# Optimization experiments

Measured on AMD Instinct MI355X. Metric: run time of the kernel, lower is better.

The kernel has to match this reference:

```python
import jax, jax.numpy as jnp
import numpy as np

N = 50000          # nodes
E = 1_600_000      # edges (avg degree 32)
F_IN = 256
F_OUT = 256
ALPHA = 0.2        # LeakyReLU negative slope


def setup_inputs() -> dict:
    key = jax.random.key(0)
    ks = jax.random.split(key, 7)
    x = jax.random.normal(ks[0], (N, F_IN), dtype=jnp.float32)
    row = jax.random.randint(ks[1], (E,), 0, N, dtype=jnp.int32)  # dst i
    col = jax.random.randint(ks[2], (E,), 0, N, dtype=jnp.int32)  # src j
    W_w = jax.random.normal(ks[3], (F_IN, F_OUT), dtype=jnp.float32) / np.sqrt(F_IN).astype(np.float32)
    W_b = jax.random.normal(ks[4], (F_OUT,), dtype=jnp.float32) * 0.01
    a_w = jax.random.normal(ks[5], (2 * F_OUT,), dtype=jnp.float32) / np.sqrt(2 * F_OUT).astype(np.float32)
    a_b = jax.random.normal(ks[6], (1,), dtype=jnp.float32) * 0.01
    return {"x": x, "W_w": W_w, "W_b": W_b, "a_w": a_w, "a_b": a_b,
            "row": row, "col": col}


def reference(x, W_w, W_b, a_w, a_b, row, col):
    # Wh = W(x): [N, F_OUT]
    Wh = x @ W_w + W_b
    # e[i,j] = leakyrelu(a1 . Wh[j] + a2 . Wh[i] + b)
    # (repeat puts Wh[j] in the first half of the concat, repeat_interleave Wh[i] in the second)
    f_dst_part = Wh @ a_w[:F_OUT]   # contribution of column node j
    f_row_part = Wh @ a_w[F_OUT:]   # contribution of row node i
    e = f_dst_part[col] + f_row_part[row] + a_b[0]          # [E]
    e = jnp.where(e > 0, e, ALPHA * e)                      # LeakyReLU
    # sparse softmax over dim=1 (segment = row i), adjacency values are 1.0
    m = jax.ops.segment_max(e, row, num_segments=N)         # [N]
    ex = jnp.exp(e - m[row])
    denom = jax.ops.segment_sum(ex, row, num_segments=N)    # [N]
    att = ex / denom[row]                                   # [E]
    # h'[i] = sum_j att[i,j] * Wh[j]  (spmm), empty rows stay zero
    h_prime = jax.ops.segment_sum(att[:, None] * Wh[col], row, num_segments=N)
    return jax.nn.relu(h_prime)
```

## Files before the change

### kernel.cpp

```cpp
#include <hip/hip_runtime.h>
#include <math.h>

#define N_NODES 50000
#define N_EDGES 1600000
#define F 256
#define ALPHA 0.2f
#define NP 50048
#define NB 196
#define CAP 10240
#define EPB 4096
#define NAB ((N_EDGES + EPB - 1) / EPB)
#define UNROLL 16
#define GEMM_BLOCKS 782
#define FVEC_SLOTS 2048

typedef short bf16x8 __attribute__((ext_vector_type(8)));
typedef float f32x4 __attribute__((ext_vector_type(4)));
typedef _Float16 half4 __attribute__((ext_vector_type(4)));

__device__ __forceinline__ unsigned short f2bf(float f) {
  union { float f; unsigned u; } v; v.f = f;
  unsigned u = v.u;
  return (unsigned short)((u + 0x7fffu + ((u >> 16) & 1u)) >> 16);
}

__device__ __forceinline__ unsigned short f2h_bits(float f) {
  union { _Float16 h; unsigned short u; } v;
  v.h = (_Float16)f;
  return v.u;
}

__device__ __forceinline__ float h_bits2f(unsigned short u) {
  union { _Float16 h; unsigned short u; } v;
  v.u = u;
  return (float)v.h;
}

__global__ __launch_bounds__(256) void prep_w(const float* __restrict__ W,
                                              const float* __restrict__ a_w,
                                              const float* __restrict__ W_b,
                                              const float* __restrict__ a_b,
                                              unsigned short* __restrict__ Wt,
                                              float* __restrict__ wa,
                                              float* __restrict__ cb,
                                              int* __restrict__ gcur) {
  if (blockIdx.x == 64) {
    if (threadIdx.x < NB) gcur[threadIdx.x] = 0;
    return;
  }
  const int lane = threadIdx.x & 63, w = threadIdx.x >> 6;
  const int k = blockIdx.x * 4 + w;
  float4 wv = *(const float4*)(W + (size_t)k * F + lane * 4);
  float4 a1 = *(const float4*)(a_w + lane * 4);
  float4 a2 = *(const float4*)(a_w + F + lane * 4);
  Wt[(size_t)(lane * 4 + 0) * F + k] = f2bf(wv.x);
  Wt[(size_t)(lane * 4 + 1) * F + k] = f2bf(wv.y);
  Wt[(size_t)(lane * 4 + 2) * F + k] = f2bf(wv.z);
  Wt[(size_t)(lane * 4 + 3) * F + k] = f2bf(wv.w);
  float s1 = wv.x * a1.x + wv.y * a1.y + wv.z * a1.z + wv.w * a1.w;
  float s2 = wv.x * a2.x + wv.y * a2.y + wv.z * a2.z + wv.w * a2.w;
#pragma unroll
  for (int off = 32; off > 0; off >>= 1) {
    s1 += __shfl_down(s1, off, 64);
    s2 += __shfl_down(s2, off, 64);
  }
  if (lane == 0) { wa[k] = s1; wa[F + k] = s2; }
  if (blockIdx.x == 0 && w == 0) {
    float4 b = *(const float4*)(W_b + lane * 4);
    float t1 = b.x * (a1.x + a2.x) + b.y * (a1.y + a2.y) +
               b.z * (a1.z + a2.z) + b.w * (a1.w + a2.w);
#pragma unroll
    for (int off = 32; off > 0; off >>= 1) t1 += __shfl_down(t1, off, 64);
    if (lane == 0) cb[0] = t1 + a_b[0];
  }
}

#define LDSK 72
__global__ __launch_bounds__(256) void gemm_fvec_binA2(
    const float* __restrict__ x,
    const unsigned short* __restrict__ Wt,
    const float* __restrict__ bias,
    const float* __restrict__ wa,
    const int* __restrict__ row,
    const int* __restrict__ col,
    _Float16* __restrict__ Wh,
    float* __restrict__ f_dst,
    float* __restrict__ f_row,
    int* __restrict__ gcur,
    unsigned* __restrict__ gstage) {
  __shared__ char smem[2 * 128 * LDSK * 2];
  if (blockIdx.x < GEMM_BLOCKS) {
    short* As = (short*)smem;
    short* Bs = As + 128 * LDSK;
    const int tid = threadIdx.x;
    const int lane = tid & 63;
    const int w = tid >> 6;
    const int wm = w >> 1, wn = w & 1;
    const int m0 = (blockIdx.x >> 1) * 128;
    const int n0 = (blockIdx.x & 1) * 128;
    f32x4 acc[4][4] = {{{0.f, 0.f, 0.f, 0.f}}};
    const int srow = tid >> 3;
    const int schunk = tid & 7;
    for (int k0 = 0; k0 < F; k0 += 64) {
#pragma unroll
      for (int i = 0; i < 4; ++i) {
        int r = i * 32 + srow;
        int gm = m0 + r; if (gm > N_NODES - 1) gm = N_NODES - 1;
        const float* src = x + (size_t)gm * F + k0 + schunk * 8;
        float4 lo = *(const float4*)src;
        float4 hi = *(const float4*)(src + 4);
        bf16x8 v;
        v[0] = (short)f2bf(lo.x); v[1] = (short)f2bf(lo.y);
        v[2] = (short)f2bf(lo.z); v[3] = (short)f2bf(lo.w);
        v[4] = (short)f2bf(hi.x); v[5] = (short)f2bf(hi.y);
        v[6] = (short)f2bf(hi.z); v[7] = (short)f2bf(hi.w);
        *(bf16x8*)&As[r * LDSK + schunk * 8] = v;
        *(bf16x8*)&Bs[r * LDSK + schunk * 8] =
            *(const bf16x8*)(Wt + (size_t)(n0 + r) * F + k0 + schunk * 8);
      }
      __syncthreads();
#pragma unroll
      for (int kk = 0; kk < 64; kk += 32) {
        const int rowsel = lane & 15;
        const int ksel = kk + (lane >> 4) * 8;
        bf16x8 af[4], bfr[4];
#pragma unroll
        for (int t = 0; t < 4; ++t) {
          af[t] = *(bf16x8*)&As[(wm * 64 + t * 16 + rowsel) * LDSK + ksel];
          bfr[t] = *(bf16x8*)&Bs[(wn * 64 + t * 16 + rowsel) * LDSK + ksel];
        }
#pragma unroll
        for (int mi = 0; mi < 4; ++mi)
#pragma unroll
          for (int nj = 0; nj < 4; ++nj)
            acc[mi][nj] = __builtin_amdgcn_mfma_f32_16x16x32_bf16(
                af[mi], bfr[nj], acc[mi][nj], 0, 0, 0);
      }
      __syncthreads();
    }
    const int crow = (lane >> 4) * 4;
    const int ccol = lane & 15;
#pragma unroll
    for (int nj = 0; nj < 4; ++nj) {
      int gc = n0 + wn * 64 + nj * 16 + ccol;
      float bv = bias[gc];
#pragma unroll
      for (int mi = 0; mi < 4; ++mi) {
        int gr = m0 + wm * 64 + mi * 16 + crow;
#pragma unroll
        for (int r = 0; r < 4; ++r)
          Wh[(size_t)(gr + r) * F + gc] = (_Float16)(acc[mi][nj][r] + bv);
      }
    }
    return;
  }
  if (blockIdx.x < GEMM_BLOCKS + NAB) {
    int* h = (int*)smem;
    int* lofs = h + NB;
    int* lcur = lofs + NB;
    int* gb = lcur + NB;
    unsigned* stage = (unsigned*)(gb + NB);
    const int t = threadIdx.x;
    for (int i = t; i < NB; i += 256) { h[i] = 0; lcur[i] = 0; }
    __syncthreads();
    const int base = (blockIdx.x - GEMM_BLOCKS) * EPB;
    const int cnt = min(EPB, N_EDGES - base);
#pragma unroll
    for (int j = 0; j < 16; ++j) {
      int k = base + j * 256 + t;
      if (k < N_EDGES) atomicAdd(&h[row[k] >> 8], 1);
    }
    __syncthreads();
    if (t == 0) {
      int run = 0;
      for (int i = 0; i < NB; ++i) { lofs[i] = run; run += h[i]; }
    }
    __syncthreads();
    if (t < NB && h[t] > 0) gb[t] = atomicAdd(&gcur[t], h[t]);
    __syncthreads();
#pragma unroll
    for (int j = 0; j < 16; ++j) {
      int k = base + j * 256 + t;
      if (k < N_EDGES) {
        int r = row[k], b = r >> 8;
        int lp = lofs[b] + atomicAdd(&lcur[b], 1);
        stage[lp] = ((unsigned)b << 24) | ((unsigned)(r & 255) << 16) |
                    (unsigned)col[k];
      }
    }
    __syncthreads();
#pragma unroll
    for (int j = 0; j < 16; ++j) {
      int s = j * 256 + t;
      if (s < cnt) {
        unsigned wv = stage[s];
        int b = wv >> 24;
        gstage[(size_t)b * CAP + gb[b] + (s - lofs[b])] = wv & 0x00FFFFFFu;
      }
    }
    return;
  }
  const int lane = threadIdx.x & 63, w = threadIdx.x >> 6;
  const int slot = blockIdx.x - GEMM_BLOCKS - NAB;
  float4 v1 = *(const float4*)(wa + lane * 4);
  float4 v2 = *(const float4*)(wa + F + lane * 4);
  for (int node = slot * 4 + w; node < N_NODES; node += FVEC_SLOTS * 4) {
    float4 xv = *(const float4*)(x + (size_t)node * F + lane * 4);
    float s1 = xv.x * v1.x + xv.y * v1.y + xv.z * v1.z + xv.w * v1.w;
    float s2 = xv.x * v2.x + xv.y * v2.y + xv.z * v2.z + xv.w * v2.w;
#pragma unroll
    for (int off = 32; off > 0; off >>= 1) {
      s1 += __shfl_down(s1, off, 64);
      s2 += __shfl_down(s2, off, 64);
    }
    if (lane == 0) { f_dst[node] = s1; f_row[node] = s2; }
  }
}

__global__ __launch_bounds__(512) void binB(const int* __restrict__ gcur,
                                            const unsigned* __restrict__ gstage,
                                            const float* __restrict__ f_dst,
                                            const float* __restrict__ f_row,
                                            const float* __restrict__ cb,
                                            int2* __restrict__ rsc,
                                            float* __restrict__ inv_denom,
                                            unsigned* __restrict__ csr) {
  __shared__ int cnt2[2048];
  __shared__ int cur2[2048];
  __shared__ int rcnt[256], rbase[256];
  __shared__ float dsum[256];
  const int t = threadIdx.x;
  const int b = blockIdx.x;
  for (int i = t; i < 2048; i += 512) cnt2[i] = 0;
  if (t < 256) dsum[t] = 0.f;
  __syncthreads();
  const int nb = gcur[b];
  const int start = b * CAP;
  const float cbs = cb[0];
  for (int s = t; s < nb; s += 512) {
    unsigned wv = gstage[start + s];
    int key = (((wv >> 16) & 255) << 3) | ((wv & 0xFFFFu) >> 13);
    atomicAdd(&cnt2[key], 1);
  }
  __syncthreads();
  if (t < 256) {
    int tot = 0;
#pragma unroll
    for (int q = 0; q < 8; ++q) tot += cnt2[t * 8 + q];
    rcnt[t] = tot;
  }
  __syncthreads();
  if (t == 0) {
    int run = 0;
    for (int i = 0; i < 256; ++i) { rbase[i] = run; run += rcnt[i]; }
  }
  __syncthreads();
  if (t < 256) {
    int base = start + rbase[t];
    int g = (b << 8) + t;
    if (g < N_NODES) rsc[g] = make_int2(base, rcnt[t]);
    int run = base;
#pragma unroll
    for (int q = 0; q < 8; ++q) { cur2[t * 8 + q] = run; run += cnt2[t * 8 + q]; }
  }
  __syncthreads();
  for (int s = t; s < nb; s += 512) {
    unsigned wv = gstage[start + s];
    int lr = (wv >> 16) & 255;
    int c = wv & 0xFFFF;
    float ev = f_dst[c] + f_row[(b << 8) + lr] + cbs;
    ev = ev > 0.f ? ev : ALPHA * ev;
    float ex = __expf(ev);
    int p = atomicAdd(&cur2[(lr << 3) | (c >> 13)], 1);
    csr[p] = ((unsigned)f2h_bits(ex) << 16) | (unsigned)c;
    atomicAdd(&dsum[lr], ex);
  }
  __syncthreads();
  if (t < 256) {
    int g = (b << 8) + t;
    if (g < N_NODES) inv_denom[g] = (rcnt[t] > 0) ? (1.0f / dsum[t]) : 0.f;
  }
}

__global__ __launch_bounds__(256) void gat_pull(const int2* __restrict__ rsc,
                                                const unsigned* __restrict__ csr,
                                                const float* __restrict__ inv_denom,
                                                const _Float16* __restrict__ Wh,
                                                float* __restrict__ out) {
  const int lane = threadIdx.x & 63, w = threadIdx.x >> 6;
  const int i = blockIdx.x * 4 + w;
  if (i >= N_NODES) return;
  const int2 rc = rsc[i];
  const int s = rc.x, e = rc.x + rc.y;
  const char* whb = (const char*)Wh;
  const unsigned laneoff = (unsigned)lane * 8u;
  float4 acc = make_float4(0.f, 0.f, 0.f, 0.f);
  for (int p = s; p < e; p += UNROLL) {
    unsigned wv[UNROLL];
#pragma unroll
    for (int j = 0; j < UNROLL; ++j) {
      int q = p + j;
      wv[j] = csr[q < e ? q : s];
    }
    half4 v[UNROLL];
#pragma unroll
    for (int j = 0; j < UNROLL; ++j) {
      unsigned off = (wv[j] & 0xFFFFu) * 512u + laneoff;
      v[j] = *(const half4*)(whb + off);
    }
#pragma unroll
    for (int j = 0; j < UNROLL; ++j) {
      float xw = h_bits2f((unsigned short)(wv[j] >> 16));
      xw = (p + j < e) ? xw : 0.f;
      acc.x += xw * (float)v[j][0];
      acc.y += xw * (float)v[j][1];
      acc.z += xw * (float)v[j][2];
      acc.w += xw * (float)v[j][3];
    }
  }
  const float inv = inv_denom[i];
  acc.x = fmaxf(acc.x * inv, 0.f); acc.y = fmaxf(acc.y * inv, 0.f);
  acc.z = fmaxf(acc.z * inv, 0.f); acc.w = fmaxf(acc.w * inv, 0.f);
  ((float4*)out)[(size_t)i * 64 + lane] = acc;
}

extern "C" void kernel_launch(void* const* d_in, const int* in_sizes, int n_in,
                              void* d_out, int out_size, void* d_ws, size_t ws_size,
                              hipStream_t stream) {
  const float* x   = (const float*)d_in[0];
  const float* W_w = (const float*)d_in[1];
  const float* W_b = (const float*)d_in[2];
  const float* a_w = (const float*)d_in[3];
  const float* a_b = (const float*)d_in[4];
  const int*   row = (const int*)d_in[5];
  const int*   col = (const int*)d_in[6];
  float* out = (float*)d_out;

  float* ws = (float*)d_ws;
  size_t off = 0;
  _Float16* Wh = (_Float16*)(ws + off); off += (size_t)NP * F / 2;
  unsigned short* Wt = (unsigned short*)(ws + off); off += (F * F) / 2;
  float* wa = ws + off;            off += 2 * F;
  float* cb = ws + off;            off += 8;
  float* f_dst = ws + off;         off += NP;
  float* f_row = ws + off;         off += NP;
  int* gcur = (int*)(ws + off);    off += NB;
  int2* rsc = (int2*)(ws + off);   off += 2 * (size_t)NP;
  float* inv_denom = (float*)(ws + off); off += NP;
  unsigned* gstage = (unsigned*)(ws + off); off += (size_t)NB * CAP;
  unsigned* csr = (unsigned*)(ws + off); off += (size_t)NB * CAP;
  (void)ws_size; (void)in_sizes; (void)n_in; (void)out_size;

  hipLaunchKernelGGL(prep_w, dim3(65), dim3(256), 0, stream, W_w, a_w, W_b,
                     a_b, Wt, wa, cb, gcur);
  hipLaunchKernelGGL(gemm_fvec_binA2, dim3(GEMM_BLOCKS + NAB + FVEC_SLOTS),
                     dim3(256), 0, stream, x, Wt, W_b, wa, row, col, Wh,
                     f_dst, f_row, gcur, gstage);
  hipLaunchKernelGGL(binB, dim3(NB), dim3(512), 0, stream, gcur, gstage,
                     f_dst, f_row, cb, rsc, inv_denom, csr);
  hipLaunchKernelGGL(gat_pull, dim3((N_NODES + 3) / 4), dim3(256), 0, stream,
                     rsc, csr, inv_denom, Wh, out);
}
```

Before: 281.5 us.

## Replace per-row pull SpMM with column-sorted push into LDS row-tile accumulators

Edges inside each 256-row bin are now reordered by (64-row group, row mod 4, source-column block). Each gat_push block owns a 64-row tile accumulated in 64KB of shared memory, and each wave processes one row-mod-4 slice. Sorting by source column is meant to improve L2 locality for Wh gathers, and the per-node CSR offsets are no longer needed. In exchange, each wave walks a long sequential edge list with only 4-way unrolling and does shared-memory read-modify-write updates. Edge entries grow to 8 bytes with fp32 weights, and the large LDS footprint limits occupancy, which may reduce memory-level parallelism.

```diff
diff --git a/kernel.cpp b/kernel.cpp
--- a/kernel.cpp
+++ b/kernel.cpp
@@ -10,7 +10,6 @@
 #define CAP 10240
 #define EPB 4096
 #define NAB ((N_EDGES + EPB - 1) / EPB)
-#define UNROLL 16
 #define GEMM_BLOCKS 782
 #define FVEC_SLOTS 2048
 
@@ -22,18 +21,6 @@
   union { float f; unsigned u; } v; v.f = f;
   unsigned u = v.u;
   return (unsigned short)((u + 0x7fffu + ((u >> 16) & 1u)) >> 16);
-}
-
-__device__ __forceinline__ unsigned short f2h_bits(float f) {
-  union { _Float16 h; unsigned short u; } v;
-  v.h = (_Float16)f;
-  return v.u;
-}
-
-__device__ __forceinline__ float h_bits2f(unsigned short u) {
-  union { _Float16 h; unsigned short u; } v;
-  v.u = u;
-  return (float)v.h;
 }
 
 __global__ __launch_bounds__(256) void prep_w(const float* __restrict__ W,
@@ -222,12 +209,11 @@
                                             const float* __restrict__ f_dst,
                                             const float* __restrict__ f_row,
                                             const float* __restrict__ cb,
-                                            int2* __restrict__ rsc,
+                                            int2* __restrict__ wofs,
                                             float* __restrict__ inv_denom,
-                                            unsigned* __restrict__ csr) {
-  __shared__ int cnt2[2048];
-  __shared__ int cur2[2048];
-  __shared__ int rcnt[256], rbase[256];
+                                            uint2* __restrict__ csr2) {
+  __shared__ int cnt2[2048], cur2[2048];
+  __shared__ int psum[512];
   __shared__ float dsum[256];
   const int t = threadIdx.x;
   const int b = blockIdx.x;
@@ -239,89 +225,106 @@
   const float cbs = cb[0];
   for (int s = t; s < nb; s += 512) {
     unsigned wv = gstage[start + s];
-    int key = (((wv >> 16) & 255) << 3) | ((wv & 0xFFFFu) >> 13);
+    int lr = (wv >> 16) & 255, c = wv & 0xFFFF;
+    int key = ((lr >> 6) << 9) | ((lr & 3) << 7) | (c >> 9);
     atomicAdd(&cnt2[key], 1);
   }
   __syncthreads();
-  if (t < 256) {
-    int tot = 0;
-#pragma unroll
-    for (int q = 0; q < 8; ++q) tot += cnt2[t * 8 + q];
-    rcnt[t] = tot;
-  }
+  const int lbase = t * 4;
+  int l0 = cnt2[lbase], l1 = cnt2[lbase + 1], l2 = cnt2[lbase + 2],
+      l3 = cnt2[lbase + 3];
+  psum[t] = l0 + l1 + l2 + l3;
   __syncthreads();
   if (t == 0) {
     int run = 0;
-    for (int i = 0; i < 256; ++i) { rbase[i] = run; run += rcnt[i]; }
-  }
-  __syncthreads();
-  if (t < 256) {
-    int base = start + rbase[t];
-    int g = (b << 8) + t;
-    if (g < N_NODES) rsc[g] = make_int2(base, rcnt[t]);
-    int run = base;
-#pragma unroll
-    for (int q = 0; q < 8; ++q) { cur2[t * 8 + q] = run; run += cnt2[t * 8 + q]; }
+    for (int i = 0; i < 512; ++i) { int v = psum[i]; psum[i] = run; run += v; }
+  }
+  __syncthreads();
+  {
+    int base = start + psum[t];
+    cur2[lbase] = base;
+    cur2[lbase + 1] = base + l0;
+    cur2[lbase + 2] = base + l0 + l1;
+    cur2[lbase + 3] = base + l0 + l1 + l2;
+  }
+  __syncthreads();
+  if (t < 16) {
+    int k = ((t >> 2) << 9) | ((t & 3) << 7);
+    int s0 = cur2[k];
+    int e0 = (t == 15) ? (start + nb) : cur2[k + 128];
+    wofs[b * 16 + t] = make_int2(s0, e0);
   }
   __syncthreads();
   for (int s = t; s < nb; s += 512) {
     unsigned wv = gstage[start + s];
-    int lr = (wv >> 16) & 255;
-    int c = wv & 0xFFFF;
+    int lr = (wv >> 16) & 255, c = wv & 0xFFFF;
     float ev = f_dst[c] + f_row[(b << 8) + lr] + cbs;
     ev = ev > 0.f ? ev : ALPHA * ev;
     float ex = __expf(ev);
-    int p = atomicAdd(&cur2[(lr << 3) | (c >> 13)], 1);
-    csr[p] = ((unsigned)f2h_bits(ex) << 16) | (unsigned)c;
+    int key = ((lr >> 6) << 9) | ((lr & 3) << 7) | (c >> 9);
+    int p = atomicAdd(&cur2[key], 1);
+    csr2[p] = make_uint2((unsigned)c | ((unsigned)(lr & 63) << 16),
+                         __float_as_uint(ex));
     atomicAdd(&dsum[lr], ex);
   }
   __syncthreads();
   if (t < 256) {
     int g = (b << 8) + t;
-    if (g < N_NODES) inv_denom[g] = (rcnt[t] > 0) ? (1.0f / dsum[t]) : 0.f;
-  }
-}
-
-__global__ __launch_bounds__(256) void gat_pull(const int2* __restrict__ rsc,
-                                                const unsigned* __restrict__ csr,
+    if (g < N_NODES) inv_denom[g] = dsum[t] > 0.f ? (1.0f / dsum[t]) : 0.f;
+  }
+}
+
+__global__ __launch_bounds__(256) void gat_push(const int2* __restrict__ wofs,
+                                                const uint2* __restrict__ csr2,
                                                 const float* __restrict__ inv_denom,
                                                 const _Float16* __restrict__ Wh,
                                                 float* __restrict__ out) {
-  const int lane = threadIdx.x & 63, w = threadIdx.x >> 6;
-  const int i = blockIdx.x * 4 + w;
-  if (i >= N_NODES) return;
-  const int2 rc = rsc[i];
-  const int s = rc.x, e = rc.x + rc.y;
-  const char* whb = (const char*)Wh;
-  const unsigned laneoff = (unsigned)lane * 8u;
-  float4 acc = make_float4(0.f, 0.f, 0.f, 0.f);
-  for (int p = s; p < e; p += UNROLL) {
-    unsigned wv[UNROLL];
-#pragma unroll
-    for (int j = 0; j < UNROLL; ++j) {
+  __shared__ float acc[64 * 256];
+  const int t = threadIdx.x;
+  float4* a4 = (float4*)acc;
+  for (int i = t; i < 64 * 64; i += 256)
+    a4[i] = make_float4(0.f, 0.f, 0.f, 0.f);
+  __syncthreads();
+  const int lane = t & 63, w = t >> 6;
+  const int2 se = wofs[blockIdx.x * 4 + w];
+  const int s0 = se.x, e0 = se.y;
+  const half4* Wh4 = (const half4*)Wh;
+  for (int p = s0; p < e0; p += 4) {
+    uint2 en[4];
+#pragma unroll
+    for (int j = 0; j < 4; ++j) {
       int q = p + j;
-      wv[j] = csr[q < e ? q : s];
-    }
-    half4 v[UNROLL];
-#pragma unroll
-    for (int j = 0; j < UNROLL; ++j) {
-      unsigned off = (wv[j] & 0xFFFFu) * 512u + laneoff;
-      v[j] = *(const half4*)(whb + off);
-    }
-#pragma unroll
-    for (int j = 0; j < UNROLL; ++j) {
-      float xw = h_bits2f((unsigned short)(wv[j] >> 16));
-      xw = (p + j < e) ? xw : 0.f;
-      acc.x += xw * (float)v[j][0];
-      acc.y += xw * (float)v[j][1];
-      acc.z += xw * (float)v[j][2];
-      acc.w += xw * (float)v[j][3];
-    }
-  }
-  const float inv = inv_denom[i];
-  acc.x = fmaxf(acc.x * inv, 0.f); acc.y = fmaxf(acc.y * inv, 0.f);
-  acc.z = fmaxf(acc.z * inv, 0.f); acc.w = fmaxf(acc.w * inv, 0.f);
-  ((float4*)out)[(size_t)i * 64 + lane] = acc;
+      en[j] = csr2[q < e0 ? q : s0];
+    }
+    half4 v[4];
+#pragma unroll
+    for (int j = 0; j < 4; ++j)
+      v[j] = Wh4[(size_t)(en[j].x & 0xFFFFu) * 64 + lane];
+#pragma unroll
+    for (int j = 0; j < 4; ++j) {
+      float wgt = (p + j < e0) ? __uint_as_float(en[j].y) : 0.f;
+      int lr6 = (en[j].x >> 16) & 63;
+      float* ap = &acc[lr6 * 256 + lane * 4];
+      ap[0] += wgt * (float)v[j][0];
+      ap[1] += wgt * (float)v[j][1];
+      ap[2] += wgt * (float)v[j][2];
+      ap[3] += wgt * (float)v[j][3];
+    }
+  }
+  __syncthreads();
+  const int rowbase = ((blockIdx.x >> 2) << 8) + ((blockIdx.x & 3) << 6);
+#pragma unroll
+  for (int k = 0; k < 16; ++k) {
+    int i = k * 256 + t;
+    int grow = rowbase + (i >> 6);
+    if (grow < N_NODES) {
+      float inv = inv_denom[grow];
+      float4 v = a4[i];
+      v.x = fmaxf(v.x * inv, 0.f); v.y = fmaxf(v.y * inv, 0.f);
+      v.z = fmaxf(v.z * inv, 0.f); v.w = fmaxf(v.w * inv, 0.f);
+      ((float4*)out)[(size_t)grow * 64 + (i & 63)] = v;
+    }
+  }
 }
 
 extern "C" void kernel_launch(void* const* d_in, const int* in_sizes, int n_in,
@@ -345,10 +348,10 @@
   float* f_dst = ws + off;         off += NP;
   float* f_row = ws + off;         off += NP;
   int* gcur = (int*)(ws + off);    off += NB;
-  int2* rsc = (int2*)(ws + off);   off += 2 * (size_t)NP;
+  int2* wofs = (int2*)(ws + off);  off += 2 * NB * 16;
   float* inv_denom = (float*)(ws + off); off += NP;
   unsigned* gstage = (unsigned*)(ws + off); off += (size_t)NB * CAP;
-  unsigned* csr = (unsigned*)(ws + off); off += (size_t)NB * CAP;
+  uint2* csr2 = (uint2*)(ws + off); off += 2 * (size_t)NB * CAP;
   (void)ws_size; (void)in_sizes; (void)n_in; (void)out_size;
 
   hipLaunchKernelGGL(prep_w, dim3(65), dim3(256), 0, stream, W_w, a_w, W_b,
@@ -357,7 +360,7 @@
                      dim3(256), 0, stream, x, Wt, W_b, wa, row, col, Wh,
                      f_dst, f_row, gcur, gstage);
   hipLaunchKernelGGL(binB, dim3(NB), dim3(512), 0, stream, gcur, gstage,
-                     f_dst, f_row, cb, rsc, inv_denom, csr);
-  hipLaunchKernelGGL(gat_pull, dim3((N_NODES + 3) / 4), dim3(256), 0, stream,
-                     rsc, csr, inv_denom, Wh, out);
-}
+                     f_dst, f_row, cb, wofs, inv_denom, csr2);
+  hipLaunchKernelGGL(gat_push, dim3(NB * 4), dim3(256), 0, stream, wofs,
+                     csr2, inv_denom, Wh, out);
+}
```

Result: slower. 395.9 us (+40.6%).
